# Kernel optimization log

Measured on AMD Instinct MI355X. Metric: run time of the kernel, lower is better.

## Reference

```python
import jax, jax.numpy as jnp
import numpy as np

MAX_DEPTH = 8
LMBDA = 0.1
OUTPUT_DIM = 128


def setup_inputs() -> dict:
    key = jax.random.key(0)
    k1, k2, k3, k4, k5, k6 = jax.random.split(key, 6)
    B, D, C = 8192, 2048, OUTPUT_DIM
    n_inner = 2 ** MAX_DEPTH - 1  # 255 inner nodes, BFS order
    n_leaf = 2 ** MAX_DEPTH       # 256 leaves
    x = jax.random.normal(k1, (B, D), dtype=jnp.float32)
    target = jax.random.randint(k2, (B,), 0, C)
    # small scale so sigmoid gates are not saturated (log(pen), log(1-pen) finite)
    W = jax.random.normal(k3, (n_inner, D), dtype=jnp.float32) * 0.02
    b = jax.random.normal(k4, (n_inner,), dtype=jnp.float32) * 0.02
    beta = jax.random.normal(k5, (n_inner,), dtype=jnp.float32)
    leaf_params = jax.random.normal(k6, (n_leaf, C), dtype=jnp.float32)
    return {"x": x, "target": target, "W": W, "b": b, "beta": beta,
            "leaf_params": leaf_params}


def reference(x, target, W, b, beta, leaf_params):
    B = x.shape[0]
    C = leaf_params.shape[1]
    y = jax.nn.one_hot(target, C, dtype=x.dtype)  # target_onehot

    # All inner-node gates as one batched GEMM: p[b,i] = sigmoid(beta_i*(x@w_i+b_i))
    p = jax.nn.sigmoid(beta[None, :] * (x @ W.T + b[None, :]))  # [B, n_inner]

    # Level-by-level path probability propagation (BFS node order).
    path = jnp.ones((B, 1), x.dtype)
    penalties = []  # per-level [2^d] node penalties
    start = 0
    for d in range(MAX_DEPTH):
        n = 2 ** d
        p_lvl = p[:, start:start + n]                      # [B, 2^d]
        pen = jnp.sum(p_lvl * path, axis=0) / jnp.sum(path, axis=0)
        penalties.append(pen)
        # left child gets path*(1-p), right gets path*p; interleave -> next level
        path = jnp.stack([path * (1.0 - p_lvl), path * p_lvl], axis=-1).reshape(B, 2 * n)
        start += n
    # path: [B, n_leaf] leaf path probabilities (left-to-right order)

    Q = jax.nn.softmax(leaf_params, axis=-1)               # [n_leaf, C]
    TQ = y @ jnp.log(Q).T                                  # [B, n_leaf], y . log Q per leaf
    loss = jnp.mean(jnp.sum(path * TQ, axis=1))

    # Penalty C: only inner nodes whose children are NOT leaves contribute
    # (original get_penalty drops depth==max_depth nodes), depths 1..max_depth-1.
    Cpen = jnp.asarray(0.0, x.dtype)
    for d in range(MAX_DEPTH - 1):
        lam = LMBDA * 2.0 ** (-(d + 1))
        pen = penalties[d]
        Cpen = Cpen - lam * 0.5 * jnp.sum(jnp.log(pen) + jnp.log(1.0 - pen))

    total = -loss + Cpen

    # output: Q of the max-path-prob leaf per sample
    leaf_idx = jnp.argmax(path, axis=1)                    # [B]
    output = Q[leaf_idx]                                   # [B, C]
    return total, output
```

## Files before the change

### kernel.cpp

```cpp
#include <hip/hip_runtime.h>
#include <hip/hip_bf16.h>
#include <hip/hip_fp16.h>
#include <stdint.h>

#define B_SIZE 8192
#define D_SIZE 2048
#define C_SIZE 128
#define N_INNER 255
#define N_LEAF 256
#define NPAD 256
#define NBLK_PATH 512

typedef _Float16 half8 __attribute__((ext_vector_type(8)));
typedef __fp16 pk16x2 __attribute__((ext_vector_type(2)));
typedef float f32x4 __attribute__((ext_vector_type(4)));
typedef unsigned short u16;

__device__ inline uint32_t pkh(float a, float b) {
    pk16x2 h = __builtin_amdgcn_cvt_pkrtz(a, b);
    return __builtin_bit_cast(uint32_t, h);
}
__device__ inline void split4(const float4 v, uint2& hi, uint2& lo) {
    pk16x2 a01 = __builtin_amdgcn_cvt_pkrtz(v.x, v.y);
    pk16x2 a23 = __builtin_amdgcn_cvt_pkrtz(v.z, v.w);
    float r0 = v.x - (float)a01[0];
    float r1 = v.y - (float)a01[1];
    float r2 = v.z - (float)a23[0];
    float r3 = v.w - (float)a23[1];
    hi = make_uint2(__builtin_bit_cast(uint32_t, a01), __builtin_bit_cast(uint32_t, a23));
    lo = make_uint2(pkh(r0, r1), pkh(r2, r3));
}

__global__ __launch_bounds__(256) void split_w_kernel(
    const float* __restrict__ Wsrc, u16* __restrict__ Wh, u16* __restrict__ Wl)
{
    int row = blockIdx.x;
    int t = threadIdx.x;
    int k = t * 8;
    uint2 h0, l0, h1, l1;
    if (row < N_INNER) {
        float4 v0 = *(const float4*)(Wsrc + (size_t)row * D_SIZE + k);
        float4 v1 = *(const float4*)(Wsrc + (size_t)row * D_SIZE + k + 4);
        split4(v0, h0, l0); split4(v1, h1, l1);
    } else {
        h0 = l0 = h1 = l1 = make_uint2(0u, 0u);
    }
    *(uint2*)&Wh[(size_t)row * D_SIZE + k]     = h0;
    *(uint2*)&Wh[(size_t)row * D_SIZE + k + 4] = h1;
    *(uint2*)&Wl[(size_t)row * D_SIZE + k]     = l0;
    *(uint2*)&Wl[(size_t)row * D_SIZE + k + 4] = l1;
}

__global__ __launch_bounds__(128) void softmax_kernel(
    const float* __restrict__ lp, float* __restrict__ Q, float* __restrict__ logQt)
{
    int row = blockIdx.x;
    int t = threadIdx.x;
    __shared__ float red[128];
    float v = lp[row * C_SIZE + t];
    red[t] = v; __syncthreads();
    for (int s = 64; s > 0; s >>= 1) { if (t < s) red[t] = fmaxf(red[t], red[t + s]); __syncthreads(); }
    float mx = red[0]; __syncthreads();
    float e = expf(v - mx);
    red[t] = e; __syncthreads();
    for (int s = 64; s > 0; s >>= 1) { if (t < s) red[t] += red[t + s]; __syncthreads(); }
    float sum = red[0];
    Q[row * C_SIZE + t] = e / sum;
    logQt[(size_t)t * N_LEAF + row] = (v - mx) - logf(sum);
}

#define GBM 64
#define GBK 32
#define GKSPLIT 4
#define KCHUNK (D_SIZE / GKSPLIT)
#define KITERS (KCHUNK / GBK)
#define LDKA 40

__global__ __launch_bounds__(256, 2) void gemm_mfma(
    const float* __restrict__ x, const u16* __restrict__ Wh, const u16* __restrict__ Wl,
    float* __restrict__ zp)
{
    __shared__ __align__(16) u16 sAh[GBM * LDKA];
    __shared__ __align__(16) u16 sAl[GBM * LDKA];

    const int t = threadIdx.x;
    const int lane = t & 63, w = t >> 6;
    const int lr = lane & 15, lq = lane >> 4;
    const int m0 = blockIdx.x * GBM;
    const int kz = blockIdx.z;

    f32x4 acc[4][4];
    #pragma unroll
    for (int mt = 0; mt < 4; ++mt)
        #pragma unroll
        for (int nt = 0; nt < 4; ++nt) acc[mt][nt] = (f32x4){0.f, 0.f, 0.f, 0.f};

    const int arow0 = t >> 3, akq = t & 7;
    const int kb0 = kz * KCHUNK;

    float4 av0 = *(const float4*)(x + (size_t)(m0 + arow0) * D_SIZE + kb0 + akq * 4);
    float4 av1 = *(const float4*)(x + (size_t)(m0 + 32 + arow0) * D_SIZE + kb0 + akq * 4);

    for (int kt = 0; kt < KITERS; ++kt) {
        const int kb = kb0 + kt * GBK;
        __syncthreads();
        {
            uint2 hi, lo;
            split4(av0, hi, lo);
            *(uint2*)&sAh[arow0 * LDKA + akq * 4] = hi;
            *(uint2*)&sAl[arow0 * LDKA + akq * 4] = lo;
            split4(av1, hi, lo);
            *(uint2*)&sAh[(arow0 + 32) * LDKA + akq * 4] = hi;
            *(uint2*)&sAl[(arow0 + 32) * LDKA + akq * 4] = lo;
        }
        __syncthreads();
        if (kt + 1 < KITERS) {
            av0 = *(const float4*)(x + (size_t)(m0 + arow0) * D_SIZE + kb + GBK + akq * 4);
            av1 = *(const float4*)(x + (size_t)(m0 + 32 + arow0) * D_SIZE + kb + GBK + akq * 4);
        }
        half8 bh[4], bl[4];
        #pragma unroll
        for (int nt = 0; nt < 4; ++nt) {
            int row = w * 64 + nt * 16 + lr;
            const u16* src = Wh + (size_t)row * D_SIZE + kb + lq * 8;
            bh[nt] = *(const half8*)src;
            const u16* srcl = Wl + (size_t)row * D_SIZE + kb + lq * 8;
            bl[nt] = *(const half8*)srcl;
        }
        half8 ah[4], al[4];
        #pragma unroll
        for (int mt = 0; mt < 4; ++mt) {
            int off = (mt * 16 + lr) * LDKA + lq * 8;
            ah[mt] = *(const half8*)&sAh[off];
            al[mt] = *(const half8*)&sAl[off];
        }
        #pragma unroll
        for (int mt = 0; mt < 4; ++mt)
            #pragma unroll
            for (int nt = 0; nt < 4; ++nt) {
                acc[mt][nt] = __builtin_amdgcn_mfma_f32_16x16x32_f16(ah[mt], bh[nt], acc[mt][nt], 0, 0, 0);
                acc[mt][nt] = __builtin_amdgcn_mfma_f32_16x16x32_f16(ah[mt], bl[nt], acc[mt][nt], 0, 0, 0);
                acc[mt][nt] = __builtin_amdgcn_mfma_f32_16x16x32_f16(al[mt], bh[nt], acc[mt][nt], 0, 0, 0);
            }
    }

    float* zout = zp + (size_t)kz * B_SIZE * NPAD;
    #pragma unroll
    for (int mt = 0; mt < 4; ++mt) {
        #pragma unroll
        for (int nt = 0; nt < 4; ++nt) {
            int gn = w * 64 + nt * 16 + lr;
            #pragma unroll
            for (int r = 0; r < 4; ++r) {
                int gm = m0 + mt * 16 + lq * 4 + r;
                zout[(size_t)gm * NPAD + gn] = acc[mt][nt][r];
            }
        }
    }
}

__global__ __launch_bounds__(256) void path_kernel(
    const float* __restrict__ z, const int* __restrict__ target,
    const float* __restrict__ bvec, const float* __restrict__ beta,
    const float* __restrict__ Q, const float* __restrict__ logQt,
    float* __restrict__ partial, float* __restrict__ out)
{
    __shared__ float pbuf[4][256];
    __shared__ float s_num[128], s_den[128], s_loss;
    const int t = threadIdx.x, w = t >> 6, lane = t & 63;
    const int c0 = lane * 4;
    float pnum[4] = {0.f, 0.f, 0.f, 0.f};
    float pden[4] = {0.f, 0.f, 0.f, 0.f};
    float loss = 0.f;

    if (t < 128) s_num[t] = 0.f;
    else s_den[t - 128] = 0.f;
    if (t == 0) s_loss = 0.f;

    float bet[4], bia[4];
    #pragma unroll
    for (int j = 0; j < 4; ++j) {
        int c = c0 + j;
        bet[j] = (c < N_INNER) ? beta[c] : 0.f;
        bia[j] = (c < N_INNER) ? bvec[c] : 0.f;
    }

    for (int i = 0; i < 4; ++i) {
        int r = blockIdx.x * 16 + w * 4 + i;
        float4 s = make_float4(0.f, 0.f, 0.f, 0.f);
        #pragma unroll
        for (int p = 0; p < GKSPLIT; ++p) {
            float4 v = *(const float4*)(z + ((size_t)p * B_SIZE + r) * NPAD + c0);
            s.x += v.x; s.y += v.y; s.z += v.z; s.w += v.w;
        }
        float zv[4] = {s.x, s.y, s.z, s.w};
        float pv[4];
        #pragma unroll
        for (int j = 0; j < 4; ++j) {
            int c = c0 + j;
            pv[j] = (c < N_INNER) ? 1.f / (1.f + expf(-bet[j] * (zv[j] + bia[j]))) : 0.f;
        }
        *(float4*)&pbuf[w][c0] = make_float4(pv[0], pv[1], pv[2], pv[3]);
        __syncthreads();

        int tg = target[r];
        float4 lq4 = *(const float4*)(logQt + (size_t)tg * N_LEAF + c0);
        float lqa[4] = {lq4.x, lq4.y, lq4.z, lq4.w};
        float lsum = 0.f, bestV = -1.f;
        int bestI = 0;
        #pragma unroll
        for (int j = 0; j < 4; ++j) {
            int leaf = c0 + j;
            float pl = 1.f;
            #pragma unroll
            for (int d = 0; d < 8; ++d) {
                int node = (1 << d) - 1 + (leaf >> (8 - d));
                int bit = (leaf >> (7 - d)) & 1;
                float pvn = pbuf[w][node];
                pl *= bit ? pvn : (1.f - pvn);
            }
            lsum += pl * lqa[j];
            if (pl > bestV) { bestV = pl; bestI = leaf; }
        }
        if (lane < 32) {
            #pragma unroll
            for (int j = 0; j < 4; ++j) {
                int c = c0 + j;
                if (c < 127) {
                    int h = c + 1; int d = 31 - __clz(h);
                    float pp = 1.f;
                    for (int e = 0; e < d; ++e) {
                        int ha = h >> (d - e);
                        int bit = (h >> (d - 1 - e)) & 1;
                        float pvn = pbuf[w][ha - 1];
                        pp *= bit ? pvn : (1.f - pvn);
                    }
                    pnum[j] += pbuf[w][c] * pp;
                    pden[j] += pp;
                }
            }
        }
        #pragma unroll
        for (int m = 1; m < 64; m <<= 1) {
            lsum += __shfl_xor(lsum, m, 64);
            float ov = __shfl_xor(bestV, m, 64);
            int   oi = __shfl_xor(bestI, m, 64);
            if (ov > bestV || (ov == bestV && oi < bestI)) { bestV = ov; bestI = oi; }
        }
        loss += lsum;
        out[1 + (size_t)r * C_SIZE + lane]      = Q[bestI * C_SIZE + lane];
        out[1 + (size_t)r * C_SIZE + lane + 64] = Q[bestI * C_SIZE + lane + 64];
        __syncthreads();
    }

    if (lane < 32) {
        #pragma unroll
        for (int j = 0; j < 4; ++j) {
            int c = c0 + j;
            if (c < 127) {
                atomicAdd(&s_num[c], pnum[j]);
                atomicAdd(&s_den[c], pden[j]);
            }
        }
    }
    if (lane == 0) atomicAdd(&s_loss, loss);
    __syncthreads();
    float* rec = partial + (size_t)blockIdx.x * 256;
    if (t < 127)        rec[t] = s_num[t];
    else if (t == 127)  rec[127] = s_loss;
    else if (t < 255)   rec[t] = s_den[t - 128];
    else                rec[255] = 0.f;
}

__global__ __launch_bounds__(256) void reduce_kernel(
    const float* __restrict__ partial, float* __restrict__ out)
{
    __shared__ float s[256];
    __shared__ float red[128];
    int t = threadIdx.x;
    float a0 = 0.f, a1 = 0.f, a2 = 0.f, a3 = 0.f;
    for (int r = 0; r < NBLK_PATH; r += 4) {
        a0 += partial[(size_t)(r + 0) * 256 + t];
        a1 += partial[(size_t)(r + 1) * 256 + t];
        a2 += partial[(size_t)(r + 2) * 256 + t];
        a3 += partial[(size_t)(r + 3) * 256 + t];
    }
    s[t] = (a0 + a1) + (a2 + a3);
    __syncthreads();
    float term = 0.f;
    if (t < 127) {
        int d = 31 - __clz(t + 1);
        float lam = 0.1f * exp2f(-(float)(d + 1));
        float pen = s[t] / s[128 + t];
        term = lam * 0.5f * (logf(pen) + logf(1.f - pen));
    }
    if (t < 128) { red[t] = term; }
    __syncthreads();
    for (int sh = 64; sh > 0; sh >>= 1) { if (t < sh) red[t] += red[t + sh]; __syncthreads(); }
    if (t == 0) out[0] = -(s[127] / (float)B_SIZE) - red[0];
}

extern "C" void kernel_launch(void* const* d_in, const int* in_sizes, int n_in,
                              void* d_out, int out_size, void* d_ws, size_t ws_size,
                              hipStream_t stream)
{
    const float* x    = (const float*)d_in[0];
    const int*   tgt  = (const int*)d_in[1];
    const float* W    = (const float*)d_in[2];
    const float* b    = (const float*)d_in[3];
    const float* beta = (const float*)d_in[4];
    const float* lp   = (const float*)d_in[5];
    float* out = (float*)d_out;

    float* z     = (float*)d_ws;
    float* Q     = z + (size_t)GKSPLIT * B_SIZE * NPAD;
    float* logQt = Q + (size_t)N_LEAF * C_SIZE;
    u16*   Wh    = (u16*)(logQt + (size_t)C_SIZE * N_LEAF);
    u16*   Wl    = Wh + (size_t)N_LEAF * D_SIZE;
    float* partial = (float*)(Wl + (size_t)N_LEAF * D_SIZE);

    split_w_kernel<<<N_LEAF, 256, 0, stream>>>(W, Wh, Wl);
    softmax_kernel<<<N_LEAF, 128, 0, stream>>>(lp, Q, logQt);

    dim3 ggrid(B_SIZE / GBM, 1, GKSPLIT);
    gemm_mfma<<<ggrid, 256, 0, stream>>>(x, Wh, Wl, z);

    path_kernel<<<NBLK_PATH, 256, 0, stream>>>(
        z, tgt, b, beta, Q, logQt, partial, out);

    reduce_kernel<<<1, 256, 0, stream>>>(partial, out);
}
```

Baseline: 184.6 us.

## Give each GEMM wave a private LDS A-tile and drop block barriers

New measurement: 180.7 us. -2.1%, faster.

```diff
diff --git a/kernel.cpp b/kernel.cpp
--- a/kernel.cpp
+++ b/kernel.cpp
@@ -31,42 +31,45 @@
     lo = make_uint2(pkh(r0, r1), pkh(r2, r3));
 }
 
-__global__ __launch_bounds__(256) void split_w_kernel(
-    const float* __restrict__ Wsrc, u16* __restrict__ Wh, u16* __restrict__ Wl)
-{
-    int row = blockIdx.x;
+__global__ __launch_bounds__(256) void prep_kernel(
+    const float* __restrict__ Wsrc, u16* __restrict__ Wh, u16* __restrict__ Wl,
+    const float* __restrict__ lp, float* __restrict__ Q, float* __restrict__ logQt)
+{
+    int bid = blockIdx.x;
     int t = threadIdx.x;
-    int k = t * 8;
-    uint2 h0, l0, h1, l1;
-    if (row < N_INNER) {
-        float4 v0 = *(const float4*)(Wsrc + (size_t)row * D_SIZE + k);
-        float4 v1 = *(const float4*)(Wsrc + (size_t)row * D_SIZE + k + 4);
-        split4(v0, h0, l0); split4(v1, h1, l1);
+    if (bid < 256) {
+        int row = bid;
+        int k = t * 8;
+        uint2 h0, l0, h1, l1;
+        if (row < N_INNER) {
+            float4 v0 = *(const float4*)(Wsrc + (size_t)row * D_SIZE + k);
+            float4 v1 = *(const float4*)(Wsrc + (size_t)row * D_SIZE + k + 4);
+            split4(v0, h0, l0); split4(v1, h1, l1);
+        } else {
+            h0 = l0 = h1 = l1 = make_uint2(0u, 0u);
+        }
+        *(uint2*)&Wh[(size_t)row * D_SIZE + k]     = h0;
+        *(uint2*)&Wh[(size_t)row * D_SIZE + k + 4] = h1;
+        *(uint2*)&Wl[(size_t)row * D_SIZE + k]     = l0;
+        *(uint2*)&Wl[(size_t)row * D_SIZE + k + 4] = l1;
     } else {
-        h0 = l0 = h1 = l1 = make_uint2(0u, 0u);
-    }
-    *(uint2*)&Wh[(size_t)row * D_SIZE + k]     = h0;
-    *(uint2*)&Wh[(size_t)row * D_SIZE + k + 4] = h1;
-    *(uint2*)&Wl[(size_t)row * D_SIZE + k]     = l0;
-    *(uint2*)&Wl[(size_t)row * D_SIZE + k + 4] = l1;
-}
-
-__global__ __launch_bounds__(128) void softmax_kernel(
-    const float* __restrict__ lp, float* __restrict__ Q, float* __restrict__ logQt)
-{
-    int row = blockIdx.x;
-    int t = threadIdx.x;
-    __shared__ float red[128];
-    float v = lp[row * C_SIZE + t];
-    red[t] = v; __syncthreads();
-    for (int s = 64; s > 0; s >>= 1) { if (t < s) red[t] = fmaxf(red[t], red[t + s]); __syncthreads(); }
-    float mx = red[0]; __syncthreads();
-    float e = expf(v - mx);
-    red[t] = e; __syncthreads();
-    for (int s = 64; s > 0; s >>= 1) { if (t < s) red[t] += red[t + s]; __syncthreads(); }
-    float sum = red[0];
-    Q[row * C_SIZE + t] = e / sum;
-    logQt[(size_t)t * N_LEAF + row] = (v - mx) - logf(sum);
+        int row = bid - 256;
+        __shared__ float red[128];
+        float v = 0.f;
+        if (t < 128) { v = lp[row * C_SIZE + t]; red[t] = v; }
+        __syncthreads();
+        for (int s = 64; s > 0; s >>= 1) { if (t < s) red[t] = fmaxf(red[t], red[t + s]); __syncthreads(); }
+        float mx = red[0]; __syncthreads();
+        float e = 0.f;
+        if (t < 128) { e = expf(v - mx); red[t] = e; }
+        __syncthreads();
+        for (int s = 64; s > 0; s >>= 1) { if (t < s) red[t] += red[t + s]; __syncthreads(); }
+        float sum = red[0];
+        if (t < 128) {
+            Q[row * C_SIZE + t] = e / sum;
+            logQt[(size_t)t * N_LEAF + row] = (v - mx) - logf(sum);
+        }
+    }
 }
 
 #define GBM 64
@@ -80,14 +83,15 @@
     const float* __restrict__ x, const u16* __restrict__ Wh, const u16* __restrict__ Wl,
     float* __restrict__ zp)
 {
-    __shared__ __align__(16) u16 sAh[GBM * LDKA];
-    __shared__ __align__(16) u16 sAl[GBM * LDKA];
+    __shared__ __align__(16) u16 sAh[4][GBM * LDKA];
+    __shared__ __align__(16) u16 sAl[4][GBM * LDKA];
 
     const int t = threadIdx.x;
     const int lane = t & 63, w = t >> 6;
     const int lr = lane & 15, lq = lane >> 4;
     const int m0 = blockIdx.x * GBM;
     const int kz = blockIdx.z;
+    const int kb0 = kz * KCHUNK;
 
     f32x4 acc[4][4];
     #pragma unroll
@@ -95,44 +99,48 @@
         #pragma unroll
         for (int nt = 0; nt < 4; ++nt) acc[mt][nt] = (f32x4){0.f, 0.f, 0.f, 0.f};
 
-    const int arow0 = t >> 3, akq = t & 7;
-    const int kb0 = kz * KCHUNK;
-
-    float4 av0 = *(const float4*)(x + (size_t)(m0 + arow0) * D_SIZE + kb0 + akq * 4);
-    float4 av1 = *(const float4*)(x + (size_t)(m0 + 32 + arow0) * D_SIZE + kb0 + akq * 4);
-
+    float4 av_c[8];
+    #pragma unroll
+    for (int i = 0; i < 8; ++i) {
+        int idx = i * 64 + lane;
+        int row = idx >> 3, ch = idx & 7;
+        av_c[i] = *(const float4*)(x + (size_t)(m0 + row) * D_SIZE + kb0 + ch * 4);
+    }
+
+    #pragma unroll
     for (int kt = 0; kt < KITERS; ++kt) {
         const int kb = kb0 + kt * GBK;
-        __syncthreads();
-        {
-            uint2 hi, lo;
-            split4(av0, hi, lo);
-            *(uint2*)&sAh[arow0 * LDKA + akq * 4] = hi;
-            *(uint2*)&sAl[arow0 * LDKA + akq * 4] = lo;
-            split4(av1, hi, lo);
-            *(uint2*)&sAh[(arow0 + 32) * LDKA + akq * 4] = hi;
-            *(uint2*)&sAl[(arow0 + 32) * LDKA + akq * 4] = lo;
-        }
-        __syncthreads();
-        if (kt + 1 < KITERS) {
-            av0 = *(const float4*)(x + (size_t)(m0 + arow0) * D_SIZE + kb + GBK + akq * 4);
-            av1 = *(const float4*)(x + (size_t)(m0 + 32 + arow0) * D_SIZE + kb + GBK + akq * 4);
-        }
         half8 bh[4], bl[4];
         #pragma unroll
         for (int nt = 0; nt < 4; ++nt) {
             int row = w * 64 + nt * 16 + lr;
-            const u16* src = Wh + (size_t)row * D_SIZE + kb + lq * 8;
-            bh[nt] = *(const half8*)src;
-            const u16* srcl = Wl + (size_t)row * D_SIZE + kb + lq * 8;
-            bl[nt] = *(const half8*)srcl;
-        }
+            bh[nt] = *(const half8*)(Wh + (size_t)row * D_SIZE + kb + lq * 8);
+            bl[nt] = *(const half8*)(Wl + (size_t)row * D_SIZE + kb + lq * 8);
+        }
+        float4 av_n[8];
+        if (kt + 1 < KITERS) {
+            #pragma unroll
+            for (int i = 0; i < 8; ++i) {
+                int idx = i * 64 + lane;
+                int row = idx >> 3, ch = idx & 7;
+                av_n[i] = *(const float4*)(x + (size_t)(m0 + row) * D_SIZE + kb + GBK + ch * 4);
+            }
+        }
+        #pragma unroll
+        for (int i = 0; i < 8; ++i) {
+            int idx = i * 64 + lane;
+            int row = idx >> 3, ch = idx & 7;
+            uint2 hi, lo; split4(av_c[i], hi, lo);
+            *(uint2*)&sAh[w][row * LDKA + ch * 4] = hi;
+            *(uint2*)&sAl[w][row * LDKA + ch * 4] = lo;
+        }
+        asm volatile("s_waitcnt lgkmcnt(0)" ::: "memory");
         half8 ah[4], al[4];
         #pragma unroll
         for (int mt = 0; mt < 4; ++mt) {
             int off = (mt * 16 + lr) * LDKA + lq * 8;
-            ah[mt] = *(const half8*)&sAh[off];
-            al[mt] = *(const half8*)&sAl[off];
+            ah[mt] = *(const half8*)&sAh[w][off];
+            al[mt] = *(const half8*)&sAl[w][off];
         }
         #pragma unroll
         for (int mt = 0; mt < 4; ++mt)
@@ -142,6 +150,10 @@
                 acc[mt][nt] = __builtin_amdgcn_mfma_f32_16x16x32_f16(ah[mt], bl[nt], acc[mt][nt], 0, 0, 0);
                 acc[mt][nt] = __builtin_amdgcn_mfma_f32_16x16x32_f16(al[mt], bh[nt], acc[mt][nt], 0, 0, 0);
             }
+        if (kt + 1 < KITERS) {
+            #pragma unroll
+            for (int i = 0; i < 8; ++i) av_c[i] = av_n[i];
+        }
     }
 
     float* zout = zp + (size_t)kz * B_SIZE * NPAD;
@@ -176,6 +188,7 @@
     if (t < 128) s_num[t] = 0.f;
     else s_den[t - 128] = 0.f;
     if (t == 0) s_loss = 0.f;
+    __syncthreads();
 
     float bet[4], bia[4];
     #pragma unroll
@@ -201,7 +214,7 @@
             pv[j] = (c < N_INNER) ? 1.f / (1.f + expf(-bet[j] * (zv[j] + bia[j]))) : 0.f;
         }
         *(float4*)&pbuf[w][c0] = make_float4(pv[0], pv[1], pv[2], pv[3]);
-        __syncthreads();
+        asm volatile("s_waitcnt lgkmcnt(0)" ::: "memory");
 
         int tg = target[r];
         float4 lq4 = *(const float4*)(logQt + (size_t)tg * N_LEAF + c0);
@@ -250,7 +263,7 @@
         loss += lsum;
         out[1 + (size_t)r * C_SIZE + lane]      = Q[bestI * C_SIZE + lane];
         out[1 + (size_t)r * C_SIZE + lane + 64] = Q[bestI * C_SIZE + lane + 64];
-        __syncthreads();
+        asm volatile("" ::: "memory");
     }
 
     if (lane < 32) {
@@ -319,8 +332,7 @@
     u16*   Wl    = Wh + (size_t)N_LEAF * D_SIZE;
     float* partial = (float*)(Wl + (size_t)N_LEAF * D_SIZE);
 
-    split_w_kernel<<<N_LEAF, 256, 0, stream>>>(W, Wh, Wl);
-    softmax_kernel<<<N_LEAF, 128, 0, stream>>>(lp, Q, logQt);
+    prep_kernel<<<512, 256, 0, stream>>>(W, Wh, Wl, lp, Q, logQt);
 
     dim3 ggrid(B_SIZE / GBM, 1, GKSPLIT);
     gemm_mfma<<<ggrid, 256, 0, stream>>>(x, Wh, Wl, z);
```
